# Kernel tuning notes

Measured on AMD Instinct MI355X. Metric: run time of the kernel, lower is better.

The kernel has to match this reference:

```python
import jax, jax.numpy as jnp
import numpy as np

D_MODEL = 1024
NHEAD = 16
D_K = D_MODEL // NHEAD


def setup_inputs() -> dict:
    key = jax.random.key(0)
    ks = jax.random.split(key, 9)
    s = 1.0 / np.sqrt(D_MODEL)
    return {
        "x": jax.random.normal(ks[0], (4, 2048, D_MODEL), dtype=jnp.float32),
        "Wq": jax.random.uniform(ks[1], (D_MODEL, D_MODEL), jnp.float32, -s, s),
        "bq": jax.random.uniform(ks[2], (D_MODEL,), jnp.float32, -s, s),
        "Wk": jax.random.uniform(ks[3], (D_MODEL, D_MODEL), jnp.float32, -s, s),
        "bk": jax.random.uniform(ks[4], (D_MODEL,), jnp.float32, -s, s),
        "Wv": jax.random.uniform(ks[5], (D_MODEL, D_MODEL), jnp.float32, -s, s),
        "bv": jax.random.uniform(ks[6], (D_MODEL,), jnp.float32, -s, s),
        "Wo": jax.random.uniform(ks[7], (D_MODEL, D_MODEL), jnp.float32, -s, s),
        "bo": jax.random.uniform(ks[8], (D_MODEL,), jnp.float32, -s, s),
    }


def reference(x, Wq, bq, Wk, bk, Wv, bv, Wo, bo):
    B, S, D = x.shape
    H, dk = NHEAD, D_K

    def split_heads(t):  # [B,S,D] -> [B,H,S,dk]
        return t.reshape(B, S, H, dk).transpose(0, 2, 1, 3)

    q = split_heads(x @ Wq + bq)
    k = split_heads(x @ Wk + bk)
    v = split_heads(x @ Wv + bv)

    scores = jnp.einsum('bhqd,bhkd->bhqk', q, k) / jnp.sqrt(jnp.float32(dk))
    attn = jax.nn.softmax(scores, axis=-1)
    out = jnp.einsum('bhqk,bhkd->bhqd', attn, v)  # [B,H,S,dk]
    out = out.transpose(0, 2, 1, 3).reshape(B, S, D)
    return out @ Wo + bo
```

## Files before the change

kernel.cpp:

```cpp
#include <hip/hip_runtime.h>


typedef short short8 __attribute__((ext_vector_type(8)));
typedef float f32x4 __attribute__((ext_vector_type(4)));
typedef float f32x16 __attribute__((ext_vector_type(16)));

#define DMODEL 1024
#define NH 16
#define DK 64
#define SEQ 2048
#define NB 4
#define MTOT (NB*SEQ)

__device__ __forceinline__ unsigned short f2bf(float f) {
    union { float f; unsigned u; } v; v.f = f;
    unsigned r = (v.u + 0x7FFFu + ((v.u >> 16) & 1u)) >> 16;
    return (unsigned short)r;
}

__device__ __forceinline__ unsigned pk2(float a, float b) {
    unsigned r;
    asm("v_cvt_pk_bf16_f32 %0, %1, %2" : "=v"(r) : "v"(a), "v"(b));
    return r;
}

union Frag { short8 s8; unsigned u[4]; };

__global__ __launch_bounds__(256) void cvt_kernel(const float* __restrict__ in,
                                                  short* __restrict__ out, int n4) {
    int i = blockIdx.x * 256 + threadIdx.x;
    if (i >= n4) return;
    float4 v = ((const float4*)in)[i];
    short4 o;
    o.x = (short)f2bf(v.x); o.y = (short)f2bf(v.y);
    o.z = (short)f2bf(v.z); o.w = (short)f2bf(v.w);
    ((short4*)out)[i] = o;
}

__global__ __launch_bounds__(256) void transpose_kernel(const float* __restrict__ W,
                                                        short* __restrict__ Wt) {
    __shared__ float t[32][33];
    int r0 = blockIdx.y * 32, c0 = blockIdx.x * 32;
    int tr = threadIdx.x >> 3;
    int tc = (threadIdx.x & 7) * 4;
    float4 v = *(const float4*)&W[(r0 + tr) * DMODEL + c0 + tc];
    t[tr][tc + 0] = v.x; t[tr][tc + 1] = v.y; t[tr][tc + 2] = v.z; t[tr][tc + 3] = v.w;
    __syncthreads();
    short4 o;
    o.x = (short)f2bf(t[tc + 0][tr]);
    o.y = (short)f2bf(t[tc + 1][tr]);
    o.z = (short)f2bf(t[tc + 2][tr]);
    o.w = (short)f2bf(t[tc + 3][tr]);
    *(short4*)&Wt[(c0 + tr) * DMODEL + r0 + tc] = o;
}

template<int MODE>
__global__ __launch_bounds__(256) void gemm_kernel(
    const short* __restrict__ A, const short* __restrict__ Bt,
    const float* __restrict__ b0, const float* __restrict__ b1, const float* __restrict__ b2,
    short* __restrict__ Qb, short* __restrict__ Kb, short* __restrict__ Vtb,
    float* __restrict__ Cout)
{
    __shared__ short As[128 * 72];
    __shared__ short Bs[128 * 72];
    const int K = DMODEL;
    int m0 = blockIdx.y * 128, n0 = blockIdx.x * 128;
    int tid = threadIdx.x, lane = tid & 63, wid = tid >> 6;
    int wm = (wid >> 1) * 64, wn = (wid & 1) * 64;

    f32x4 acc[4][4];
    #pragma unroll
    for (int i = 0; i < 4; i++)
        #pragma unroll
        for (int j = 0; j < 4; j++) acc[i][j] = (f32x4){0.f, 0.f, 0.f, 0.f};

    for (int kt = 0; kt < K; kt += 64) {
        #pragma unroll
        for (int i = 0; i < 4; ++i) {
            int ch = tid + 256 * i;
            int row = ch >> 3, c8 = (ch & 7) * 8;
            *(short8*)&As[row * 72 + c8] = *(const short8*)&A[(m0 + row) * K + kt + c8];
            *(short8*)&Bs[row * 72 + c8] = *(const short8*)&Bt[(n0 + row) * K + kt + c8];
        }
        __syncthreads();
        #pragma unroll
        for (int kk = 0; kk < 2; ++kk) {
            int ko = kk * 32 + (lane >> 4) * 8;
            short8 af[4], bfv[4];
            #pragma unroll
            for (int i = 0; i < 4; i++)
                af[i] = *(const short8*)&As[(wm + i * 16 + (lane & 15)) * 72 + ko];
            #pragma unroll
            for (int j = 0; j < 4; j++)
                bfv[j] = *(const short8*)&Bs[(wn + j * 16 + (lane & 15)) * 72 + ko];
            #pragma unroll
            for (int i = 0; i < 4; i++)
                #pragma unroll
                for (int j = 0; j < 4; j++)
                    acc[i][j] = __builtin_amdgcn_mfma_f32_16x16x32_bf16(af[i], bfv[j], acc[i][j], 0, 0, 0);
        }
        __syncthreads();
    }

    #pragma unroll
    for (int i = 0; i < 4; i++) {
        #pragma unroll
        for (int j = 0; j < 4; j++) {
            int col = n0 + wn + j * 16 + (lane & 15);
            #pragma unroll
            for (int r = 0; r < 4; r++) {
                int row = m0 + wm + i * 16 + (lane >> 4) * 4 + r;
                float v = acc[i][j][r];
                if (MODE == 0) {
                    int seg = col >> 10, c = col & 1023;
                    const float* bp = (seg == 0) ? b0 : (seg == 1 ? b1 : b2);
                    v += bp[c];
                    unsigned short bv = f2bf(v);
                    int hh = c >> 6, d = c & 63, bb = row >> 11, s = row & 2047;
                    if (seg == 0)      Qb [(((bb * NH + hh) * SEQ) + s) * DK + d] = (short)bv;
                    else if (seg == 1) Kb [(((bb * NH + hh) * SEQ) + s) * DK + d] = (short)bv;
                    else               Vtb[(((bb * NH + hh) * DK) + d) * SEQ + s] = (short)bv;
                } else {
                    Cout[row * DMODEL + col] = v + b0[col];
                }
            }
        }
    }
}

__global__ __launch_bounds__(256) void attn_kernel(
    const short* __restrict__ Qb, const short* __restrict__ Kb,
    const short* __restrict__ Vtb, short* __restrict__ AOb)
{
    __shared__ __align__(16) short Ks[64 * 64];
    __shared__ __align__(16) short Vs[64 * 64];
    char* ksb = (char*)Ks;
    char* vsb = (char*)Vs;

    int bid = blockIdx.x;
    int wk = (bid & 7) * 128 + (bid >> 3);
    int qi = wk & 15, bh = wk >> 4;
    int h = bh & (NH - 1), b = bh >> 4;
    int q0 = qi * 128;

    int tid = threadIdx.x, lane = tid & 63, wid = tid >> 6;
    int hi = lane >> 5, l31 = lane & 31, l7 = lane & 7;
    const short* Qp = Qb + (size_t)bh * SEQ * DK;
    const short* Kp = Kb + (size_t)bh * SEQ * DK;
    const short* Vp = Vtb + (size_t)bh * DK * SEQ;

    short8 qf[4];
    #pragma unroll
    for (int ks = 0; ks < 4; ks++)
        qf[ks] = *(const short8*)&Qp[(q0 + wid * 32 + l31) * DK + ks * 16 + hi * 8];

    f32x16 ot0, ot1;
    #pragma unroll
    for (int r = 0; r < 16; r++) { ot0[r] = 0.f; ot1[r] = 0.f; }
    float mrun = -1e30f, lrun = 0.f;

    int srow = tid >> 3, ssl = tid & 7;
    #pragma unroll
    for (int i = 0; i < 2; i++) {
        int row = srow + 32 * i;
        *(short8*)(ksb + ((row * 128 + ssl * 16) ^ ((row & 7) << 4))) =
            *(const short8*)&Kp[row * DK + ssl * 8];
        *(short8*)(vsb + ((row * 128 + ssl * 16) ^ ((row & 7) << 4))) =
            *(const short8*)&Vp[row * SEQ + ssl * 8];
    }
    __syncthreads();

    const int NT = SEQ / 64;
    for (int t = 0; t < NT; ++t) {
        short8 nk[2], nv[2];
        if (t + 1 < NT) {
            int kv0n = (t + 1) * 64;
            #pragma unroll
            for (int i = 0; i < 2; i++) {
                int row = srow + 32 * i;
                nk[i] = *(const short8*)&Kp[(kv0n + row) * DK + ssl * 8];
                nv[i] = *(const short8*)&Vp[row * SEQ + kv0n + ssl * 8];
            }
        }

        f32x16 st0, st1;
        #pragma unroll
        for (int r = 0; r < 16; r++) { st0[r] = 0.f; st1[r] = 0.f; }
        __builtin_amdgcn_s_setprio(1);
        #pragma unroll
        for (int ks = 0; ks < 4; ks++) {
            short8 kf0 = *(const short8*)(ksb + (((l31) * 128 + ks * 32 + hi * 16) ^ (l7 << 4)));
            short8 kf1 = *(const short8*)(ksb + (((32 + l31) * 128 + ks * 32 + hi * 16) ^ (l7 << 4)));
            st0 = __builtin_amdgcn_mfma_f32_32x32x16_bf16(kf0, qf[ks], st0, 0, 0, 0);
            st1 = __builtin_amdgcn_mfma_f32_32x32x16_bf16(kf1, qf[ks], st1, 0, 0, 0);
        }
        __builtin_amdgcn_s_setprio(0);

        const float SCL = 0.125f;
        #pragma unroll
        for (int r = 0; r < 16; r++) { st0[r] *= SCL; st1[r] *= SCL; }
        float mx[16];
        #pragma unroll
        for (int r = 0; r < 16; r++) mx[r] = fmaxf(st0[r], st1[r]);
        #pragma unroll
        for (int s = 8; s > 0; s >>= 1)
            #pragma unroll
            for (int r = 0; r < 8; r++) if (r < s) mx[r] = fmaxf(mx[r], mx[r + s]);
        float mt = fmaxf(mx[0], __shfl_xor(mx[0], 32, 64));
        if (!__all(mt - mrun <= 8.f)) {
            float mn = fmaxf(mrun, mt);
            float al = __expf(mrun - mn);
            lrun *= al;
            #pragma unroll
            for (int r = 0; r < 16; r++) { ot0[r] *= al; ot1[r] *= al; }
            mrun = mn;
        }
        float sm[16];
        #pragma unroll
        for (int r = 0; r < 16; r++) {
            st0[r] = __expf(st0[r] - mrun);
            st1[r] = __expf(st1[r] - mrun);
            sm[r] = st0[r] + st1[r];
        }
        #pragma unroll
        for (int s = 8; s > 0; s >>= 1)
            #pragma unroll
            for (int r = 0; r < 8; r++) if (r < s) sm[r] += sm[r + s];
        lrun += sm[0] + __shfl_xor(sm[0], 32, 64);

        unsigned w0[8], w1[8];
        #pragma unroll
        for (int m = 0; m < 4; m++) {
            w0[m * 2]     = pk2(st0[4 * m], st0[4 * m + 1]);
            w0[m * 2 + 1] = pk2(st0[4 * m + 2], st0[4 * m + 3]);
            w1[m * 2]     = pk2(st1[4 * m], st1[4 * m + 1]);
            w1[m * 2 + 1] = pk2(st1[4 * m + 2], st1[4 * m + 3]);
        }
        short8 pf[4];
        #pragma unroll
        for (int pp = 0; pp < 2; pp++) {
            {
                unsigned o0 = hi ? w0[(2 * pp + 1) * 2]     : w0[(2 * pp) * 2];
                unsigned o1 = hi ? w0[(2 * pp + 1) * 2 + 1] : w0[(2 * pp) * 2 + 1];
                unsigned s0 = hi ? w0[(2 * pp) * 2]         : w0[(2 * pp + 1) * 2];
                unsigned s1 = hi ? w0[(2 * pp) * 2 + 1]     : w0[(2 * pp + 1) * 2 + 1];
                unsigned r0 = (unsigned)__shfl_xor((int)s0, 32, 64);
                unsigned r1 = (unsigned)__shfl_xor((int)s1, 32, 64);
                Frag f;
                f.u[0] = hi ? r0 : o0; f.u[1] = hi ? r1 : o1;
                f.u[2] = hi ? o0 : r0; f.u[3] = hi ? o1 : r1;
                pf[pp] = f.s8;
            }
            {
                unsigned o0 = hi ? w1[(2 * pp + 1) * 2]     : w1[(2 * pp) * 2];
                unsigned o1 = hi ? w1[(2 * pp + 1) * 2 + 1] : w1[(2 * pp) * 2 + 1];
                unsigned s0 = hi ? w1[(2 * pp) * 2]         : w1[(2 * pp + 1) * 2];
                unsigned s1 = hi ? w1[(2 * pp) * 2 + 1]     : w1[(2 * pp + 1) * 2 + 1];
                unsigned r0 = (unsigned)__shfl_xor((int)s0, 32, 64);
                unsigned r1 = (unsigned)__shfl_xor((int)s1, 32, 64);
                Frag f;
                f.u[0] = hi ? r0 : o0; f.u[1] = hi ? r1 : o1;
                f.u[2] = hi ? o0 : r0; f.u[3] = hi ? o1 : r1;
                pf[2 + pp] = f.s8;
            }
        }

        __builtin_amdgcn_s_setprio(1);
        #pragma unroll
        for (int ks = 0; ks < 4; ks++) {
            short8 vf0 = *(const short8*)(vsb + (((l31) * 128 + ks * 32 + hi * 16) ^ (l7 << 4)));
            short8 vf1 = *(const short8*)(vsb + (((32 + l31) * 128 + ks * 32 + hi * 16) ^ (l7 << 4)));
            ot0 = __builtin_amdgcn_mfma_f32_32x32x16_bf16(vf0, pf[ks], ot0, 0, 0, 0);
            ot1 = __builtin_amdgcn_mfma_f32_32x32x16_bf16(vf1, pf[ks], ot1, 0, 0, 0);
        }
        __builtin_amdgcn_s_setprio(0);

        __syncthreads();
        if (t + 1 < NT) {
            #pragma unroll
            for (int i = 0; i < 2; i++) {
                int row = srow + 32 * i;
                *(short8*)(ksb + ((row * 128 + ssl * 16) ^ ((row & 7) << 4))) = nk[i];
                *(short8*)(vsb + ((row * 128 + ssl * 16) ^ ((row & 7) << 4))) = nv[i];
            }
        }
        __syncthreads();
    }

    float inv = 1.f / lrun;
    int srow_q = b * SEQ + q0 + wid * 32 + l31;
    short* outp = AOb + (size_t)srow_q * DMODEL + h * DK;
    #pragma unroll
    for (int g = 0; g < 4; g++) {
        int d0 = 8 * g + 4 * hi;
        uint2 u;
        u.x = pk2(ot0[4 * g] * inv, ot0[4 * g + 1] * inv);
        u.y = pk2(ot0[4 * g + 2] * inv, ot0[4 * g + 3] * inv);
        *(uint2*)&outp[d0] = u;
        uint2 v2;
        v2.x = pk2(ot1[4 * g] * inv, ot1[4 * g + 1] * inv);
        v2.y = pk2(ot1[4 * g + 2] * inv, ot1[4 * g + 3] * inv);
        *(uint2*)&outp[32 + d0] = v2;
    }
}

extern "C" void kernel_launch(void* const* d_in, const int* in_sizes, int n_in,
                              void* d_out, int out_size, void* d_ws, size_t ws_size,
                              hipStream_t stream)
{
    const float* x  = (const float*)d_in[0];
    const float* Wq = (const float*)d_in[1];
    const float* bq = (const float*)d_in[2];
    const float* Wk = (const float*)d_in[3];
    const float* bk = (const float*)d_in[4];
    const float* Wv = (const float*)d_in[5];
    const float* bv = (const float*)d_in[6];
    const float* Wo = (const float*)d_in[7];
    const float* bo = (const float*)d_in[8];
    float* out = (float*)d_out;

    char* w = (char*)d_ws;
    short* xb    = (short*)w; w += (size_t)MTOT * DMODEL * 2;
    short* Wqkvt = (short*)w; w += (size_t)3 * DMODEL * DMODEL * 2;
    short* Wot   = (short*)w; w += (size_t)DMODEL * DMODEL * 2;
    short* Qb    = (short*)w; w += (size_t)MTOT * DMODEL * 2;
    short* Kb    = (short*)w; w += (size_t)MTOT * DMODEL * 2;
    short* Vtb   = (short*)w; w += (size_t)MTOT * DMODEL * 2;
    short* AOb   = (short*)w; w += (size_t)MTOT * DMODEL * 2;

    cvt_kernel<<<(MTOT * DMODEL / 4 + 255) / 256, 256, 0, stream>>>(x, xb, MTOT * DMODEL / 4);

    dim3 tg(32, 32);
    transpose_kernel<<<tg, 256, 0, stream>>>(Wq, Wqkvt);
    transpose_kernel<<<tg, 256, 0, stream>>>(Wk, Wqkvt + DMODEL * DMODEL);
    transpose_kernel<<<tg, 256, 0, stream>>>(Wv, Wqkvt + 2 * DMODEL * DMODEL);
    transpose_kernel<<<tg, 256, 0, stream>>>(Wo, Wot);

    gemm_kernel<0><<<dim3(3 * DMODEL / 128, MTOT / 128), 256, 0, stream>>>(
        xb, Wqkvt, bq, bk, bv, Qb, Kb, Vtb, nullptr);

    attn_kernel<<<dim3(SEQ / 128 * NH * NB), 256, 0, stream>>>(Qb, Kb, Vtb, AOb);

    gemm_kernel<1><<<dim3(DMODEL / 128, MTOT / 128), 256, 0, stream>>>(
        AOb, Wot, bo, nullptr, nullptr, nullptr, nullptr, nullptr, out);
}
```

Measured before the change: 259.3 us.

## Use async LDS loads in GEMM and cheaper exp2/max3/permlane softmax in attention

The GEMM tile load now uses global_load_lds direct-to-LDS copies with an XOR-swizzled unpadded layout instead of loading through registers into padded shared memory. The K projection is pre-scaled by log2(e)/sqrt(dk) so attention can use raw v_exp_f32 (exp2) without a per-element scale multiply. Row-max reduction uses v_max3, the rescale threshold is raised, and the P fragment transpose uses v_permlane32_swap instead of cross-lane shuffles. These changes target VGPR/VALU overhead in softmax and load latency in the projection GEMMs. The risks are bf16 rounding of the pre-scaled K and a looser rescale threshold.

```diff
diff --git a/kernel.cpp b/kernel.cpp
--- a/kernel.cpp
+++ b/kernel.cpp
@@ -11,6 +11,7 @@
 #define SEQ 2048
 #define NB 4
 #define MTOT (NB*SEQ)
+#define KSCALE 0.18033688f
 
 __device__ __forceinline__ unsigned short f2bf(float f) {
     union { float f; unsigned u; } v; v.f = f;
@@ -22,6 +23,25 @@
     unsigned r;
     asm("v_cvt_pk_bf16_f32 %0, %1, %2" : "=v"(r) : "v"(a), "v"(b));
     return r;
+}
+
+__device__ __forceinline__ float exp2a(float x) {
+    float r; asm("v_exp_f32 %0, %1" : "=v"(r) : "v"(x)); return r;
+}
+
+__device__ __forceinline__ float max3a(float a, float b, float c) {
+    float r; asm("v_max3_f32 %0, %1, %2, %3" : "=v"(r) : "v"(a), "v"(b), "v"(c)); return r;
+}
+
+__device__ __forceinline__ void plswap(unsigned &a, unsigned &b) {
+    asm volatile("v_permlane32_swap_b32 %0, %1" : "+v"(a), "+v"(b));
+}
+
+__device__ __forceinline__ void gload16(const short* g, short* l) {
+    __builtin_amdgcn_global_load_lds(
+        (const __attribute__((address_space(1))) unsigned*)(const void*)g,
+        (__attribute__((address_space(3))) unsigned*)(void*)l,
+        16, 0, 0);
 }
 
 union Frag { short8 s8; unsigned u[4]; };
@@ -61,13 +81,18 @@
     short* __restrict__ Qb, short* __restrict__ Kb, short* __restrict__ Vtb,
     float* __restrict__ Cout)
 {
-    __shared__ short As[128 * 72];
-    __shared__ short Bs[128 * 72];
+    __shared__ __align__(16) short As[128 * 64];
+    __shared__ __align__(16) short Bs[128 * 64];
     const int K = DMODEL;
     int m0 = blockIdx.y * 128, n0 = blockIdx.x * 128;
     int tid = threadIdx.x, lane = tid & 63, wid = tid >> 6;
     int wm = (wid >> 1) * 64, wn = (wid & 1) * 64;
 
+    int srow = 8 * wid + (lane >> 3);
+    int scol = ((lane & 7) ^ (lane >> 3)) * 8;
+    const short* aSrc = A + (size_t)(m0 + srow) * K + scol;
+    const short* bSrc = Bt + (size_t)(n0 + srow) * K + scol;
+
     f32x4 acc[4][4];
     #pragma unroll
     for (int i = 0; i < 4; i++)
@@ -77,10 +102,8 @@
     for (int kt = 0; kt < K; kt += 64) {
         #pragma unroll
         for (int i = 0; i < 4; ++i) {
-            int ch = tid + 256 * i;
-            int row = ch >> 3, c8 = (ch & 7) * 8;
-            *(short8*)&As[row * 72 + c8] = *(const short8*)&A[(m0 + row) * K + kt + c8];
-            *(short8*)&Bs[row * 72 + c8] = *(const short8*)&Bt[(n0 + row) * K + kt + c8];
+            gload16(aSrc + (size_t)(32 * i) * K + kt, &As[(8 * wid + 32 * i) * 64]);
+            gload16(bSrc + (size_t)(32 * i) * K + kt, &Bs[(8 * wid + 32 * i) * 64]);
         }
         __syncthreads();
         #pragma unroll
@@ -88,11 +111,15 @@
             int ko = kk * 32 + (lane >> 4) * 8;
             short8 af[4], bfv[4];
             #pragma unroll
-            for (int i = 0; i < 4; i++)
-                af[i] = *(const short8*)&As[(wm + i * 16 + (lane & 15)) * 72 + ko];
-            #pragma unroll
-            for (int j = 0; j < 4; j++)
-                bfv[j] = *(const short8*)&Bs[(wn + j * 16 + (lane & 15)) * 72 + ko];
+            for (int i = 0; i < 4; i++) {
+                int r = wm + i * 16 + (lane & 15);
+                af[i] = *(const short8*)&As[(r * 64 + ko) ^ ((r & 7) << 3)];
+            }
+            #pragma unroll
+            for (int j = 0; j < 4; j++) {
+                int r = wn + j * 16 + (lane & 15);
+                bfv[j] = *(const short8*)&Bs[(r * 64 + ko) ^ ((r & 7) << 3)];
+            }
             #pragma unroll
             for (int i = 0; i < 4; i++)
                 #pragma unroll
@@ -115,6 +142,7 @@
                     int seg = col >> 10, c = col & 1023;
                     const float* bp = (seg == 0) ? b0 : (seg == 1 ? b1 : b2);
                     v += bp[c];
+                    if (seg == 1) v *= KSCALE;
                     unsigned short bv = f2bf(v);
                     int hh = c >> 6, d = c & 63, bb = row >> 11, s = row & 2047;
                     if (seg == 0)      Qb [(((bb * NH + hh) * SEQ) + s) * DK + d] = (short)bv;
@@ -189,44 +217,46 @@
         __builtin_amdgcn_s_setprio(1);
         #pragma unroll
         for (int ks = 0; ks < 4; ks++) {
-            short8 kf0 = *(const short8*)(ksb + (((l31) * 128 + ks * 32 + hi * 16) ^ (l7 << 4)));
+            short8 kf0 = *(const short8*)(ksb + ((l31 * 128 + ks * 32 + hi * 16) ^ (l7 << 4)));
             short8 kf1 = *(const short8*)(ksb + (((32 + l31) * 128 + ks * 32 + hi * 16) ^ (l7 << 4)));
             st0 = __builtin_amdgcn_mfma_f32_32x32x16_bf16(kf0, qf[ks], st0, 0, 0, 0);
             st1 = __builtin_amdgcn_mfma_f32_32x32x16_bf16(kf1, qf[ks], st1, 0, 0, 0);
         }
         __builtin_amdgcn_s_setprio(0);
 
-        const float SCL = 0.125f;
-        #pragma unroll
-        for (int r = 0; r < 16; r++) { st0[r] *= SCL; st1[r] *= SCL; }
-        float mx[16];
-        #pragma unroll
-        for (int r = 0; r < 16; r++) mx[r] = fmaxf(st0[r], st1[r]);
-        #pragma unroll
-        for (int s = 8; s > 0; s >>= 1)
-            #pragma unroll
-            for (int r = 0; r < 8; r++) if (r < s) mx[r] = fmaxf(mx[r], mx[r + s]);
-        float mt = fmaxf(mx[0], __shfl_xor(mx[0], 32, 64));
-        if (!__all(mt - mrun <= 8.f)) {
+        float m8[8];
+        #pragma unroll
+        for (int i = 0; i < 8; i++) m8[i] = max3a(st0[i], st0[i + 8], st1[i]);
+        float m4[4];
+        #pragma unroll
+        for (int i = 0; i < 4; i++) m4[i] = max3a(m8[i], m8[i + 4], st1[i + 8]);
+        float m2a = max3a(m4[0], m4[2], st1[12]);
+        float m2b = max3a(m4[1], m4[3], st1[13]);
+        float mxv = max3a(m2a, m2b, st1[14]);
+        mxv = fmaxf(mxv, st1[15]);
+        float mt = fmaxf(mxv, __shfl_xor(mxv, 32, 64));
+
+        if (!__all(mt - mrun <= 11.0f)) {
             float mn = fmaxf(mrun, mt);
-            float al = __expf(mrun - mn);
+            float al = exp2a(mrun - mn);
             lrun *= al;
             #pragma unroll
             for (int r = 0; r < 16; r++) { ot0[r] *= al; ot1[r] *= al; }
             mrun = mn;
         }
-        float sm[16];
         #pragma unroll
         for (int r = 0; r < 16; r++) {
-            st0[r] = __expf(st0[r] - mrun);
-            st1[r] = __expf(st1[r] - mrun);
-            sm[r] = st0[r] + st1[r];
-        }
+            st0[r] = exp2a(st0[r] - mrun);
+            st1[r] = exp2a(st1[r] - mrun);
+        }
+        float s16[16];
+        #pragma unroll
+        for (int r = 0; r < 16; r++) s16[r] = st0[r] + st1[r];
         #pragma unroll
         for (int s = 8; s > 0; s >>= 1)
             #pragma unroll
-            for (int r = 0; r < 8; r++) if (r < s) sm[r] += sm[r + s];
-        lrun += sm[0] + __shfl_xor(sm[0], 32, 64);
+            for (int r = 0; r < 8; r++) if (r < s) s16[r] += s16[r + s];
+        lrun += s16[0] + __shfl_xor(s16[0], 32, 64);
 
         unsigned w0[8], w1[8];
         #pragma unroll
@@ -238,37 +268,22 @@
         }
         short8 pf[4];
         #pragma unroll
-        for (int pp = 0; pp < 2; pp++) {
-            {
-                unsigned o0 = hi ? w0[(2 * pp + 1) * 2]     : w0[(2 * pp) * 2];
-                unsigned o1 = hi ? w0[(2 * pp + 1) * 2 + 1] : w0[(2 * pp) * 2 + 1];
-                unsigned s0 = hi ? w0[(2 * pp) * 2]         : w0[(2 * pp + 1) * 2];
-                unsigned s1 = hi ? w0[(2 * pp) * 2 + 1]     : w0[(2 * pp + 1) * 2 + 1];
-                unsigned r0 = (unsigned)__shfl_xor((int)s0, 32, 64);
-                unsigned r1 = (unsigned)__shfl_xor((int)s1, 32, 64);
-                Frag f;
-                f.u[0] = hi ? r0 : o0; f.u[1] = hi ? r1 : o1;
-                f.u[2] = hi ? o0 : r0; f.u[3] = hi ? o1 : r1;
-                pf[pp] = f.s8;
-            }
-            {
-                unsigned o0 = hi ? w1[(2 * pp + 1) * 2]     : w1[(2 * pp) * 2];
-                unsigned o1 = hi ? w1[(2 * pp + 1) * 2 + 1] : w1[(2 * pp) * 2 + 1];
-                unsigned s0 = hi ? w1[(2 * pp) * 2]         : w1[(2 * pp + 1) * 2];
-                unsigned s1 = hi ? w1[(2 * pp) * 2 + 1]     : w1[(2 * pp + 1) * 2 + 1];
-                unsigned r0 = (unsigned)__shfl_xor((int)s0, 32, 64);
-                unsigned r1 = (unsigned)__shfl_xor((int)s1, 32, 64);
-                Frag f;
-                f.u[0] = hi ? r0 : o0; f.u[1] = hi ? r1 : o1;
-                f.u[2] = hi ? o0 : r0; f.u[3] = hi ? o1 : r1;
-                pf[2 + pp] = f.s8;
-            }
+        for (int ks = 0; ks < 4; ks++) {
+            unsigned a0 = (ks < 2) ? w0[4 * (ks & 1) + 0] : w1[4 * (ks & 1) + 0];
+            unsigned b0_ = (ks < 2) ? w0[4 * (ks & 1) + 2] : w1[4 * (ks & 1) + 2];
+            unsigned a1 = (ks < 2) ? w0[4 * (ks & 1) + 1] : w1[4 * (ks & 1) + 1];
+            unsigned b1_ = (ks < 2) ? w0[4 * (ks & 1) + 3] : w1[4 * (ks & 1) + 3];
+            plswap(a0, b0_);
+            plswap(a1, b1_);
+            Frag f;
+            f.u[0] = a0; f.u[1] = a1; f.u[2] = b0_; f.u[3] = b1_;
+            pf[ks] = f.s8;
         }
 
         __builtin_amdgcn_s_setprio(1);
         #pragma unroll
         for (int ks = 0; ks < 4; ks++) {
-            short8 vf0 = *(const short8*)(vsb + (((l31) * 128 + ks * 32 + hi * 16) ^ (l7 << 4)));
+            short8 vf0 = *(const short8*)(vsb + ((l31 * 128 + ks * 32 + hi * 16) ^ (l7 << 4)));
             short8 vf1 = *(const short8*)(vsb + (((32 + l31) * 128 + ks * 32 + hi * 16) ^ (l7 << 4)));
             ot0 = __builtin_amdgcn_mfma_f32_32x32x16_bf16(vf0, pf[ks], ot0, 0, 0, 0);
             ot1 = __builtin_amdgcn_mfma_f32_32x32x16_bf16(vf1, pf[ks], ot1, 0, 0, 0);
```

Result: faster. 226.3 us (-12.7%).
